# Kernel tuning notes

Hardware: AMD Instinct MI355X
Metric: run time of the kernel (lower is better)

The kernel has to match this reference:

```python
import jax, jax.numpy as jnp
import numpy as np


def setup_inputs() -> dict:
    key = jax.random.key(0)
    k1, k2 = jax.random.split(key)
    B, N, M, D = 4, 8192, 8192, 3
    prediction = jax.random.normal(k1, (B, N, D), dtype=jnp.float32)
    target = jax.random.normal(k2, (B, M, D), dtype=jnp.float32)
    return {"prediction": prediction, "target": target}


def reference(prediction, target):
    # prediction: [B, N, 3], target: [B, M, 3] (already channels-last,
    # matching the module's transpose-if-needed behavior).
    x2 = jnp.sum(prediction * prediction, axis=-1)  # [B, N]
    y2 = jnp.sum(target * target, axis=-1)          # [B, M]
    xy = jnp.einsum('bnd,bmd->bnm', prediction, target)  # [B, N, M]
    d2 = x2[:, :, None] + y2[:, None, :] - 2.0 * xy
    d2 = jnp.maximum(d2, 0.0)  # numerical guard
    # pytorch3d chamfer_distance defaults: point_reduction='mean',
    # batch_reduction='mean' -> mean over points per direction, mean over batch,
    # then sum the two directions.
    cham_x = jnp.min(d2, axis=2).mean()  # pred -> target
    cham_y = jnp.min(d2, axis=1).mean()  # target -> pred
    return cham_x + cham_y
```

## Files before the change

kernel.cpp:

```cpp
#include <hip/hip_runtime.h>


#define BLOCK 256
#define RPT 8
#define MC  256

__global__ __launch_bounds__(256) void init_min_kernel(unsigned int* __restrict__ buf, int n) {
    int i = blockIdx.x * blockDim.x + threadIdx.x;
    if (i < n) buf[i] = 0x7f800000u;
}

__global__ __launch_bounds__(BLOCK) void chamfer_min_kernel(
    const float* __restrict__ X,
    const float* __restrict__ Y,
    unsigned int* __restrict__ rowmin,
    int NX, int NY) {
    __shared__ float4 ldsY[MC];

    const int b  = blockIdx.z;
    const int mc = blockIdx.y;

    for (int p = threadIdx.x; p < MC; p += BLOCK) {
        const float* yp = Y + ((size_t)b * NY + (size_t)mc * MC + p) * 3;
        float yx = yp[0], yy = yp[1], yz = yp[2];
        ldsY[p] = make_float4(yx, yy, yz, yx * yx + yy * yy + yz * yz);
    }
    __syncthreads();

    const int row0 = blockIdx.x * (BLOCK * RPT);
    float qx[RPT], qy[RPT], qz[RPT], x2[RPT], best[RPT];
#pragma unroll
    for (int r = 0; r < RPT; ++r) {
        int row = row0 + r * BLOCK + threadIdx.x;
        const float* xp = X + ((size_t)b * NX + row) * 3;
        float px = xp[0], py = xp[1], pz = xp[2];
        qx[r] = -2.0f * px;
        qy[r] = -2.0f * py;
        qz[r] = -2.0f * pz;
        x2[r] = px * px + py * py + pz * pz;
        best[r] = 3.0e38f;
    }

#pragma unroll 4
    for (int m = 0; m < MC; ++m) {
        float4 T = ldsY[m];
#pragma unroll
        for (int r = 0; r < RPT; ++r) {
            float cand = fmaf(qx[r], T.x, fmaf(qy[r], T.y, fmaf(qz[r], T.z, T.w)));
            best[r] = fminf(best[r], cand);
        }
    }

#pragma unroll
    for (int r = 0; r < RPT; ++r) {
        int row = row0 + r * BLOCK + threadIdx.x;
        float v = fmaxf(best[r] + x2[r], 0.0f);
        atomicMin(&rowmin[(size_t)b * NX + row], __float_as_uint(v));
    }
}

__global__ __launch_bounds__(1024) void chamfer_reduce_kernel(
    const unsigned int* __restrict__ rowmin,
    const unsigned int* __restrict__ colmin,
    float* __restrict__ out, int BN, int BM) {
    double v = 0.0;
    for (int i = threadIdx.x; i < BN; i += 1024)
        v += (double)__uint_as_float(rowmin[i]) / (double)BN;
    for (int i = threadIdx.x; i < BM; i += 1024)
        v += (double)__uint_as_float(colmin[i]) / (double)BM;

    for (int off = 32; off > 0; off >>= 1) v += __shfl_down(v, off);
    __shared__ double sh[16];
    int lane = threadIdx.x & 63, wid = threadIdx.x >> 6;
    if (lane == 0) sh[wid] = v;
    __syncthreads();
    if (threadIdx.x == 0) {
        double s = 0.0;
        for (int w = 0; w < 16; ++w) s += sh[w];
        out[0] = (float)s;
    }
}

extern "C" void kernel_launch(void* const* d_in, const int* in_sizes, int n_in,
                              void* d_out, int out_size, void* d_ws, size_t ws_size,
                              hipStream_t stream) {
    const float* pred = (const float*)d_in[0];
    const float* targ = (const float*)d_in[1];
    float* out = (float*)d_out;

    const int B = 4, N = 8192, M = 8192;

    unsigned int* rowmin = (unsigned int*)d_ws;
    unsigned int* colmin = rowmin + (size_t)B * N;

    int tot = B * (N + M);
    init_min_kernel<<<(tot + 255) / 256, 256, 0, stream>>>(rowmin, tot);

    dim3 g1(N / (BLOCK * RPT), M / MC, B);
    chamfer_min_kernel<<<g1, BLOCK, 0, stream>>>(pred, targ, rowmin, N, M);

    dim3 g2(M / (BLOCK * RPT), N / MC, B);
    chamfer_min_kernel<<<g2, BLOCK, 0, stream>>>(targ, pred, colmin, M, N);

    chamfer_reduce_kernel<<<1, 1024, 0, stream>>>(rowmin, colmin, out, B * N, B * M);
}
```

Before: 121.1 us.

## Replace atomicMin row minima with partial-min buffers and parallel two-stage reduction

Each block now writes its per-chunk row minimum to a partial buffer instead of doing atomicMin into a global array. This removes the init kernel and the atomics. The single-block 1024-thread final reduction becomes a multi-block min-and-sum pass followed by a tiny final kernel. The inner loop unroll also goes from 4 to 8. In exchange it adds workspace traffic: 32 partials per row, written and then read back, about 8 MB total. The reduce kernel also assumes NCH1 equals NCH2.

After: 112.6 us. 1.08x faster.

```diff
diff --git a/kernel.cpp b/kernel.cpp
--- a/kernel.cpp
+++ b/kernel.cpp
@@ -5,20 +5,16 @@
 #define RPT 8
 #define MC  256
 
-__global__ __launch_bounds__(256) void init_min_kernel(unsigned int* __restrict__ buf, int n) {
-    int i = blockIdx.x * blockDim.x + threadIdx.x;
-    if (i < n) buf[i] = 0x7f800000u;
-}
-
-__global__ __launch_bounds__(BLOCK) void chamfer_min_kernel(
+__global__ __launch_bounds__(BLOCK) void chamfer_partial_min(
     const float* __restrict__ X,
     const float* __restrict__ Y,
-    unsigned int* __restrict__ rowmin,
+    float* __restrict__ partial,
     int NX, int NY) {
     __shared__ float4 ldsY[MC];
 
-    const int b  = blockIdx.z;
-    const int mc = blockIdx.y;
+    const int b   = blockIdx.z;
+    const int mc  = blockIdx.y;
+    const int NCH = gridDim.y;
 
     for (int p = threadIdx.x; p < MC; p += BLOCK) {
         const float* yp = Y + ((size_t)b * NY + (size_t)mc * MC + p) * 3;
@@ -41,7 +37,7 @@
         best[r] = 3.0e38f;
     }
 
-#pragma unroll 4
+#pragma unroll 8
     for (int m = 0; m < MC; ++m) {
         float4 T = ldsY[m];
 #pragma unroll
@@ -54,31 +50,53 @@
 #pragma unroll
     for (int r = 0; r < RPT; ++r) {
         int row = row0 + r * BLOCK + threadIdx.x;
-        float v = fmaxf(best[r] + x2[r], 0.0f);
-        atomicMin(&rowmin[(size_t)b * NX + row], __float_as_uint(v));
+        partial[((size_t)b * NCH + mc) * NX + row] = fmaxf(best[r] + x2[r], 0.0f);
     }
 }
 
-__global__ __launch_bounds__(1024) void chamfer_reduce_kernel(
-    const unsigned int* __restrict__ rowmin,
-    const unsigned int* __restrict__ colmin,
-    float* __restrict__ out, int BN, int BM) {
-    double v = 0.0;
-    for (int i = threadIdx.x; i < BN; i += 1024)
-        v += (double)__uint_as_float(rowmin[i]) / (double)BN;
-    for (int i = threadIdx.x; i < BM; i += 1024)
-        v += (double)__uint_as_float(colmin[i]) / (double)BM;
+__global__ __launch_bounds__(256) void chamfer_reduce_rows(
+    const float* __restrict__ pA,
+    const float* __restrict__ pB,
+    double* __restrict__ blocksum,
+    int N, int M, int B, int NCH) {
+    const int j = blockIdx.x;
+    const int nblkA = (B * N) / 256;
 
-    for (int off = 32; off > 0; off >>= 1) v += __shfl_down(v, off);
-    __shared__ double sh[16];
-    int lane = threadIdx.x & 63, wid = threadIdx.x >> 6;
-    if (lane == 0) sh[wid] = v;
+    const float* src;
+    int rows, g0;
+    if (j < nblkA) { src = pA; rows = N; g0 = j * 256; }
+    else           { src = pB; rows = M; g0 = (j - nblkA) * 256; }
+
+    const int g = g0 + threadIdx.x;
+    const int b = g / rows, r = g % rows;
+
+    float v = 3.0e38f;
+    for (int c = 0; c < NCH; ++c)
+        v = fminf(v, src[((size_t)b * NCH + c) * rows + r]);
+
+    double d = (double)v;
+    for (int off = 32; off > 0; off >>= 1) d += __shfl_down(d, off);
+    __shared__ double sh[4];
+    const int lane = threadIdx.x & 63, wid = threadIdx.x >> 6;
+    if (lane == 0) sh[wid] = d;
     __syncthreads();
-    if (threadIdx.x == 0) {
-        double s = 0.0;
-        for (int w = 0; w < 16; ++w) s += sh[w];
-        out[0] = (float)s;
-    }
+    if (threadIdx.x == 0)
+        blocksum[j] = sh[0] + sh[1] + sh[2] + sh[3];
+}
+
+__global__ __launch_bounds__(256) void chamfer_final(
+    const double* __restrict__ blocksum, float* __restrict__ out,
+    int nblkA, int nblkTot, double invBN, double invBM) {
+    const int t = threadIdx.x;
+    double d = 0.0;
+    if (t < nblkTot)
+        d = blocksum[t] * (t < nblkA ? invBN : invBM);
+    for (int off = 32; off > 0; off >>= 1) d += __shfl_down(d, off);
+    __shared__ double sh[4];
+    const int lane = t & 63, wid = t >> 6;
+    if (lane == 0) sh[wid] = d;
+    __syncthreads();
+    if (t == 0) out[0] = (float)(sh[0] + sh[1] + sh[2] + sh[3]);
 }
 
 extern "C" void kernel_launch(void* const* d_in, const int* in_sizes, int n_in,
@@ -89,18 +107,23 @@
     float* out = (float*)d_out;
 
     const int B = 4, N = 8192, M = 8192;
+    const int NCH1 = M / MC;
+    const int NCH2 = N / MC;
 
-    unsigned int* rowmin = (unsigned int*)d_ws;
-    unsigned int* colmin = rowmin + (size_t)B * N;
+    float* pA = (float*)d_ws;
+    float* pB = pA + (size_t)B * NCH1 * N;
+    double* blocksum = (double*)(pB + (size_t)B * NCH2 * M);
 
-    int tot = B * (N + M);
-    init_min_kernel<<<(tot + 255) / 256, 256, 0, stream>>>(rowmin, tot);
+    dim3 g1(N / (BLOCK * RPT), NCH1, B);
+    chamfer_partial_min<<<g1, BLOCK, 0, stream>>>(pred, targ, pA, N, M);
 
-    dim3 g1(N / (BLOCK * RPT), M / MC, B);
-    chamfer_min_kernel<<<g1, BLOCK, 0, stream>>>(pred, targ, rowmin, N, M);
+    dim3 g2(M / (BLOCK * RPT), NCH2, B);
+    chamfer_partial_min<<<g2, BLOCK, 0, stream>>>(targ, pred, pB, M, N);
 
-    dim3 g2(M / (BLOCK * RPT), N / MC, B);
-    chamfer_min_kernel<<<g2, BLOCK, 0, stream>>>(targ, pred, colmin, M, N);
+    const int nblkA = (B * N) / 256;
+    const int nblkTot = nblkA + (B * M) / 256;
+    chamfer_reduce_rows<<<nblkTot, 256, 0, stream>>>(pA, pB, blocksum, N, M, B, NCH1);
 
-    chamfer_reduce_kernel<<<1, 1024, 0, stream>>>(rowmin, colmin, out, B * N, B * M);
+    chamfer_final<<<1, 256, 0, stream>>>(blocksum, out, nblkA, nblkTot,
+                                         1.0 / ((double)B * N), 1.0 / ((double)B * M));
 }
```

## Fuse both chamfer directions into one launch and parallelize final reduction

Applied to the files above, without the earlier changes.

Merges the two direction kernels into a single grid indexed by direction and batch, doubles the target chunk size, and replaces atomicMin into a pre-initialized buffer with per-chunk partial minima written to workspace. A multi-block reduce kernel takes the min over chunks and accumulates the mean with a double atomic and a last-block ticket, removing the init kernel and the single-block reduction. It adds extra workspace traffic for partials and relies on an in-kernel reset of the accumulator.

Measured after the change: 102.3 us. 15.5% less time.

```diff
diff --git a/kernel.cpp b/kernel.cpp
--- a/kernel.cpp
+++ b/kernel.cpp
@@ -2,28 +2,35 @@
 
 
 #define BLOCK 256
-#define RPT 8
-#define MC  256
+#define RPT   8
+#define MC    512
+#define NPTS  8192
+#define NCH   (NPTS / MC)
+#define NB    4
 
-__global__ __launch_bounds__(256) void init_min_kernel(unsigned int* __restrict__ buf, int n) {
-    int i = blockIdx.x * blockDim.x + threadIdx.x;
-    if (i < n) buf[i] = 0x7f800000u;
-}
+__global__ __launch_bounds__(BLOCK) void chamfer_min_fused(
+    const float* __restrict__ pred, const float* __restrict__ targ,
+    float* __restrict__ pA,
+    float* __restrict__ pB,
+    double* __restrict__ acc, unsigned int* __restrict__ counter) {
+    if (blockIdx.x == 0 && blockIdx.y == 0 && blockIdx.z == 0 && threadIdx.x == 0) {
+        *acc = 0.0;
+        *counter = 0u;
+    }
 
-__global__ __launch_bounds__(BLOCK) void chamfer_min_kernel(
-    const float* __restrict__ X,
-    const float* __restrict__ Y,
-    unsigned int* __restrict__ rowmin,
-    int NX, int NY) {
+    const int z   = blockIdx.z;
+    const int dir = z >> 2, b = z & (NB - 1);
+    const float* X = dir ? targ : pred;
+    const float* Y = dir ? pred : targ;
+    float* partial = dir ? pB : pA;
+
     __shared__ float4 ldsY[MC];
-
-    const int b  = blockIdx.z;
     const int mc = blockIdx.y;
 
     for (int p = threadIdx.x; p < MC; p += BLOCK) {
-        const float* yp = Y + ((size_t)b * NY + (size_t)mc * MC + p) * 3;
+        const float* yp = Y + ((size_t)b * NPTS + (size_t)mc * MC + p) * 3;
         float yx = yp[0], yy = yp[1], yz = yp[2];
-        ldsY[p] = make_float4(yx, yy, yz, yx * yx + yy * yy + yz * yz);
+        ldsY[p] = make_float4(yx, yy, yz, fmaf(yx, yx, fmaf(yy, yy, yz * yz)));
     }
     __syncthreads();
 
@@ -32,52 +39,66 @@
 #pragma unroll
     for (int r = 0; r < RPT; ++r) {
         int row = row0 + r * BLOCK + threadIdx.x;
-        const float* xp = X + ((size_t)b * NX + row) * 3;
+        const float* xp = X + ((size_t)b * NPTS + row) * 3;
         float px = xp[0], py = xp[1], pz = xp[2];
         qx[r] = -2.0f * px;
         qy[r] = -2.0f * py;
         qz[r] = -2.0f * pz;
-        x2[r] = px * px + py * py + pz * pz;
+        x2[r] = fmaf(px, px, fmaf(py, py, pz * pz));
         best[r] = 3.0e38f;
     }
 
 #pragma unroll 4
-    for (int m = 0; m < MC; ++m) {
-        float4 T = ldsY[m];
+    for (int m = 0; m < MC; m += 2) {
+        float4 T0 = ldsY[m];
+        float4 T1 = ldsY[m + 1];
 #pragma unroll
         for (int r = 0; r < RPT; ++r) {
-            float cand = fmaf(qx[r], T.x, fmaf(qy[r], T.y, fmaf(qz[r], T.z, T.w)));
-            best[r] = fminf(best[r], cand);
+            float c0 = fmaf(qx[r], T0.x, fmaf(qy[r], T0.y, fmaf(qz[r], T0.z, T0.w)));
+            float c1 = fmaf(qx[r], T1.x, fmaf(qy[r], T1.y, fmaf(qz[r], T1.z, T1.w)));
+            best[r] = fminf(fminf(best[r], c0), c1);
         }
     }
 
 #pragma unroll
     for (int r = 0; r < RPT; ++r) {
         int row = row0 + r * BLOCK + threadIdx.x;
-        float v = fmaxf(best[r] + x2[r], 0.0f);
-        atomicMin(&rowmin[(size_t)b * NX + row], __float_as_uint(v));
+        partial[((size_t)b * NCH + mc) * NPTS + row] = fmaxf(best[r] + x2[r], 0.0f);
     }
 }
 
-__global__ __launch_bounds__(1024) void chamfer_reduce_kernel(
-    const unsigned int* __restrict__ rowmin,
-    const unsigned int* __restrict__ colmin,
-    float* __restrict__ out, int BN, int BM) {
-    double v = 0.0;
-    for (int i = threadIdx.x; i < BN; i += 1024)
-        v += (double)__uint_as_float(rowmin[i]) / (double)BN;
-    for (int i = threadIdx.x; i < BM; i += 1024)
-        v += (double)__uint_as_float(colmin[i]) / (double)BM;
+__global__ __launch_bounds__(256) void chamfer_reduce(
+    const float* __restrict__ pA, const float* __restrict__ pB,
+    double* __restrict__ acc, unsigned int* __restrict__ counter,
+    float* __restrict__ out) {
+    const int g = blockIdx.x * 256 + threadIdx.x;
+    const int half = NB * NPTS;
+    const float* src = (g < half) ? pA : pB;
+    const int gg = g & (half - 1);
+    const int b = gg >> 13, r = gg & (NPTS - 1);
 
-    for (int off = 32; off > 0; off >>= 1) v += __shfl_down(v, off);
-    __shared__ double sh[16];
-    int lane = threadIdx.x & 63, wid = threadIdx.x >> 6;
-    if (lane == 0) sh[wid] = v;
+    float v = 3.0e38f;
+#pragma unroll
+    for (int c = 0; c < NCH; ++c)
+        v = fminf(v, src[((size_t)b * NCH + c) * NPTS + r]);
+
+    double d = (double)v;
+    for (int off = 32; off > 0; off >>= 1) d += __shfl_down(d, off);
+    __shared__ double sh[4];
+    const int lane = threadIdx.x & 63, wid = threadIdx.x >> 6;
+    if (lane == 0) sh[wid] = d;
     __syncthreads();
+
     if (threadIdx.x == 0) {
-        double s = 0.0;
-        for (int w = 0; w < 16; ++w) s += sh[w];
-        out[0] = (float)s;
+        double blocktotal = sh[0] + sh[1] + sh[2] + sh[3];
+        atomicAdd(acc, blocktotal);
+        __threadfence();
+        unsigned int ticket = atomicAdd(counter, 1u);
+        if (ticket == gridDim.x - 1) {
+            __threadfence();
+            double s = atomicAdd(acc, 0.0);
+            out[0] = (float)(s / (double)(NB * NPTS));
+        }
     }
 }
 
@@ -88,19 +109,14 @@
     const float* targ = (const float*)d_in[1];
     float* out = (float*)d_out;
 
-    const int B = 4, N = 8192, M = 8192;
+    float* pA = (float*)d_ws;
+    float* pB = pA + (size_t)NB * NCH * NPTS;
+    double* acc = (double*)(pB + (size_t)NB * NCH * NPTS);
+    unsigned int* counter = (unsigned int*)(acc + 1);
 
-    unsigned int* rowmin = (unsigned int*)d_ws;
-    unsigned int* colmin = rowmin + (size_t)B * N;
+    dim3 g1(NPTS / (BLOCK * RPT), NCH, 2 * NB);
+    chamfer_min_fused<<<g1, BLOCK, 0, stream>>>(pred, targ, pA, pB, acc, counter);
 
-    int tot = B * (N + M);
-    init_min_kernel<<<(tot + 255) / 256, 256, 0, stream>>>(rowmin, tot);
-
-    dim3 g1(N / (BLOCK * RPT), M / MC, B);
-    chamfer_min_kernel<<<g1, BLOCK, 0, stream>>>(pred, targ, rowmin, N, M);
-
-    dim3 g2(M / (BLOCK * RPT), N / MC, B);
-    chamfer_min_kernel<<<g2, BLOCK, 0, stream>>>(targ, pred, colmin, M, N);
-
-    chamfer_reduce_kernel<<<1, 1024, 0, stream>>>(rowmin, colmin, out, B * N, B * M);
+    const int nblk = 2 * NB * NPTS / 256;
+    chamfer_reduce<<<nblk, 256, 0, stream>>>(pA, pB, acc, counter, out);
 }
```
